# Performance work log

Hardware: AMD Instinct MI355X
Metric: run time of the kernel (lower is better)

The kernel has to match this reference:

```python
import jax, jax.numpy as jnp
import numpy as np

HID = 512; HH = HID // 2; INP = 1; OUT = 1
INH = int(HID * 0.3); EXC = HID - INH            # 153 / 359
N = 3 * HH + 2 * HID + INP                       # 1793 total units
ALM_EXC_START = 3 * HH + HID                      # start of ALM excitatory block
T_CONST = 0.1; SIGMA_REC = 0.01
B, T = 128, 300


def _np_masks():
    rng = np.random.default_rng(0)
    n_zeros = int(np.ceil(0.9 * HH))
    sparse = np.ones((HH, HH), np.float32)
    for c in range(HH):
        sparse[rng.permutation(HH)[:n_zeros], c] = 0.0
    alm2str = np.concatenate([np.ones((HH, EXC), np.float32), np.zeros((HH, INH), np.float32)], 1)
    thal2d1 = np.concatenate([np.ones((HH // 2, HID), np.float32), np.zeros((HH // 2, HID), np.float32)], 0)
    alm2d1 = 1.0 - thal2d1
    iti2d1 = np.concatenate([np.ones((HH // 2, INP), np.float32), np.zeros((HH // 2, INP), np.float32)], 0)
    alm_sign = np.concatenate([np.ones(EXC, np.float32), -np.ones(INH, np.float32)])  # alm2alm_D diagonal
    return sparse, alm2str, thal2d1, alm2d1, iti2d1, alm_sign

_SPARSE, _ALM2STR, _THAL2D1M, _ALM2D1M, _ITI2D1M, _ALMSIGN = [jnp.asarray(a) for a in _np_masks()]


def _clip(w):
    return jnp.clip(w, 1e-10, 1.0)               # F.hardtanh(w, 1e-10, 1)


def _build_W(d12d1_w, d12d2_w, d22d1_w, d22d2_w, d22stn_w, d12thal_w, stn2thal_w,
             thal2alm_w, alm2alm_w, thal2d1_w, thal2d2_w, alm2d1_w, alm2d2_w,
             inp_w_d1, inp_w_d2):
    z_ss = jnp.zeros((HH, HH)); z_sl = jnp.zeros((HH, HID))
    z_ls = jnp.zeros((HID, HH)); z_ll = jnp.zeros((HID, HID))
    z_si = jnp.zeros((HH, INP)); z_li = jnp.zeros((HID, INP))
    # striatal recurrence: sparse_mask * hardtanh(w) @ (-I)
    d12d1 = -(_SPARSE * _clip(d12d1_w)); d12d2 = -(_SPARSE * _clip(d12d2_w))
    d22d1 = -(_SPARSE * _clip(d22d1_w)); d22d2 = -(_SPARSE * _clip(d22d2_w))
    row_d1 = jnp.concatenate([d12d1, d22d1, z_ss, _THAL2D1M * _clip(thal2d1_w),
                              _ALM2D1M * _ALM2STR * _clip(alm2d1_w), _ITI2D1M * _clip(inp_w_d1)], 1)
    row_d2 = jnp.concatenate([d12d2, d22d2, z_ss, _clip(thal2d2_w),
                              _ALM2STR * _clip(alm2d2_w), _clip(inp_w_d2)], 1)
    row_stn = jnp.concatenate([z_ss, _clip(d22stn_w), z_ss, z_sl, z_sl, z_si], 1)
    row_thal = jnp.concatenate([_clip(d12thal_w), z_ls, -_clip(stn2thal_w), z_ll, z_ll, z_li], 1)  # stn2thal @ (-I)
    row_alm = jnp.concatenate([z_ls, z_ls, z_ls, _clip(thal2alm_w),
                               _clip(alm2alm_w) * _ALMSIGN[None, :], z_li], 1)      # alm2alm @ D (Dale)
    row_iti = jnp.zeros((INP, N))
    return jnp.concatenate([row_d1, row_d2, row_stn, row_thal, row_alm, row_iti], 0)


def setup_inputs() -> dict:
    key = jax.random.key(0)
    ks = jax.random.split(key, 24)
    u = lambda k, s: jax.random.uniform(k, s, jnp.float32) * 0.01   # uniform(0, 0.01) init
    return {
        "inp": jax.random.uniform(ks[0], (B, T, INP), jnp.float32),
        "cue_inp": jax.random.uniform(ks[1], (B, T, INP), jnp.float32),
        "inhib_stim": jnp.zeros((B, T, N), jnp.float32),
        "hn": jax.random.uniform(ks[2], (1, B, N), jnp.float32),
        "xn": jax.random.uniform(ks[3], (1, B, N), jnp.float32),
        "noise": jax.random.normal(ks[4], (B, T, N), jnp.float32),
        "d12d1_w": u(ks[5], (HH, HH)), "d12d2_w": u(ks[6], (HH, HH)),
        "d22d1_w": u(ks[7], (HH, HH)), "d22d2_w": u(ks[8], (HH, HH)),
        "d22stn_w": u(ks[9], (HH, HH)), "d12thal_w": u(ks[10], (HID, HH)),
        "stn2thal_w": u(ks[11], (HID, HH)), "thal2alm_w": u(ks[12], (HID, HID)),
        "alm2alm_w": u(ks[13], (HID, HID)), "thal2d1_w": u(ks[14], (HH, HID)),
        "thal2d2_w": u(ks[15], (HH, HID)), "alm2d1_w": u(ks[16], (HH, HID)),
        "alm2d2_w": u(ks[17], (HH, HID)), "inp_w_d1": u(ks[18], (HH, INP)),
        "inp_w_d2": u(ks[19], (HH, INP)), "out_w_alm": u(ks[20], (OUT, EXC)),
    }


def reference(inp, cue_inp, inhib_stim, hn, xn, noise,
              d12d1_w, d12d2_w, d22d1_w, d22d2_w, d22stn_w, d12thal_w, stn2thal_w,
              thal2alm_w, alm2alm_w, thal2d1_w, thal2d2_w, alm2d1_w, alm2d2_w,
              inp_w_d1, inp_w_d2, out_w_alm):
    W = _build_W(d12d1_w, d12d2_w, d22d1_w, d22d2_w, d22stn_w, d12thal_w, stn2thal_w,
                 thal2alm_w, alm2alm_w, thal2d1_w, thal2d2_w, alm2d1_w, alm2d2_w,
                 inp_w_d1, inp_w_d2)
    # tonic current: 0.1 everywhere except ITI units
    tonic = jnp.concatenate([0.1 * jnp.ones(N - INP, jnp.float32), jnp.zeros(INP, jnp.float32)])
    seq = (inhib_stim.swapaxes(0, 1),                 # [T, B, N]
           (inp + cue_inp).swapaxes(0, 1),            # [T, B, INP] -> injected into ITI units
           noise.swapaxes(0, 1))                      # [T, B, N]

    def step(carry, s):
        x, h = carry
        inh_t, iti_t, noise_t = s
        drive = h @ W.T + tonic + inh_t + SIGMA_REC * noise_t
        drive = drive.at[:, N - INP:].add(iti_t)
        x = x + T_CONST * (-x + drive)
        h = jax.nn.relu(x)
        out = h[:, ALM_EXC_START:ALM_EXC_START + EXC] @ out_w_alm.T
        return (x, h), (h, x, out)

    (_, _), (hs, xs, outs) = jax.lax.scan(step, (xn[0], hn[0]), seq)
    return hs.swapaxes(0, 1), xs.swapaxes(0, 1), outs.swapaxes(0, 1)
```

## Files before the change

### kernel.cpp

```cpp
#include <hip/hip_runtime.h>
#include <stdint.h>
#include <string.h>

#define NREAL 1793
#define NPAD  1824
#define NROWP 1808
#define WSTR  1832
#define NBLK  113
#define NGRP  2
#define TSTEPS 300
#define BATCH 128
#define XS_OFF 68851200
#define OUT_OFF 137702400
#define LOFF (16 * WSTR)
#define LOSCALE 4096.0f
#define LOINV  2.44140625e-4f

#define ASLOT(g,i)    (((g) * 128 + (i)) * 32)

typedef _Float16 half_t;
typedef __attribute__((ext_vector_type(8))) _Float16 half8;
typedef __attribute__((ext_vector_type(4))) float f32x4;
typedef __attribute__((ext_vector_type(4))) unsigned int uint4v;

__device__ __forceinline__ float clipw(float w) {
  return fminf(fmaxf(w, 1e-10f), 1.0f);
}

__device__ __forceinline__ void store_u32_llc(unsigned int* p, unsigned int v) {
  asm volatile("global_store_dword %0, %1, off sc0 sc1"
               :: "v"((unsigned long long)(uintptr_t)p), "v"(v)
               : "memory");
}

__device__ __forceinline__ float unpack_h(uint32_t p) {
  unsigned short uh = (unsigned short)(p & 0xffffu);
  unsigned short ul = (unsigned short)(p >> 16);
  half_t hh = *(half_t*)&uh;
  half_t hl = *(half_t*)&ul;
  return (float)hh + LOINV * (float)hl;
}

__device__ __forceinline__ int rid_of(int s) {
  return (s < 8) ? 0 : (s < 16) ? 1 : (s < 32) ? 2 : (s < 48) ? 3
       : (s < 80) ? 4 : (s < 112) ? 5 : 6;
}

__device__ __forceinline__ void poll_wait(unsigned int* cnt, int g, int lane,
                                          bool in0, bool in1, bool cn0, bool cn1,
                                          unsigned tin, unsigned tcn)
{
  const int s0 = lane, s1 = lane + 64;
  for (;;) {
    unsigned a0 = __hip_atomic_load(&cnt[ASLOT(g, s0)], __ATOMIC_RELAXED,
                                    __HIP_MEMORY_SCOPE_AGENT);
    unsigned a1 = 0xFFFFFFFFu;
    if (in1 || cn1)
      a1 = __hip_atomic_load(&cnt[ASLOT(g, s1)], __ATOMIC_RELAXED,
                             __HIP_MEMORY_SCOPE_AGENT);
    unsigned vin = in0 ? a0 : 0xFFFFFFFFu;
    if (in1 && a1 < vin) vin = a1;
    unsigned vcn = cn0 ? a0 : 0xFFFFFFFFu;
    if (cn1 && a1 < vcn) vcn = a1;
    #pragma unroll
    for (int o = 32; o; o >>= 1) {
      unsigned x = __shfl_xor(vin, o); if (x < vin) vin = x;
      unsigned y = __shfl_xor(vcn, o); if (y < vcn) vcn = y;
    }
    if (vin >= tin && vcn >= tcn) break;
    __builtin_amdgcn_s_sleep(1);
  }
}

template<int LO0, int N0, int LO1, int N1, int LO2, int N2>
__device__ __forceinline__ void seg_mfma(const uint32_t* __restrict__ ap,
                                         const half_t* __restrict__ Wl, int wl_b,
                                         f32x4& acc0, f32x4& acc1, f32x4& acc2)
{
  constexpr int NC = N0 + N1 + N2;
  if constexpr (NC == 0) { return; }
  constexpr int BS = 8;
  constexpr int NB = (NC + BS - 1) / BS;
  uint4v qa0[BS], qa1[BS], qb0[BS], qb1[BS];

#define KC_OF(ci) ((ci) < N0 ? (LO0 + (ci)) : (ci) < N0 + N1 ? (LO1 + (ci) - N0) \
                              : (LO2 + (ci) - N0 - N1))

  #pragma unroll
  for (int i = 0; i < BS; ++i) {
    if (i < NC) {
      const int kc = KC_OF(i);
      qa0[i] = *(const uint4v*)(ap + kc * 32);
      qa1[i] = *(const uint4v*)(ap + kc * 32 + 4);
    }
  }
  #pragma unroll
  for (int j = 0; j < NB; ++j) {
    if (j + 1 < NB) {
      #pragma unroll
      for (int i = 0; i < BS; ++i) {
        const int ci = (j + 1) * BS + i;
        if (ci < NC) {
          const int kc = KC_OF(ci);
          if (j % 2 == 0) {
            qb0[i] = *(const uint4v*)(ap + kc * 32);
            qb1[i] = *(const uint4v*)(ap + kc * 32 + 4);
          } else {
            qa0[i] = *(const uint4v*)(ap + kc * 32);
            qa1[i] = *(const uint4v*)(ap + kc * 32 + 4);
          }
        }
      }
    }
    #pragma unroll
    for (int i = 0; i < BS; ++i) {
      const int ci = j * BS + i;
      if (ci < NC) {
        const int kc = KC_OF(ci);
        uint4v v0 = (j % 2 == 0) ? qa0[i] : qb0[i];
        uint4v v1 = (j % 2 == 0) ? qa1[i] : qb1[i];
        uint4v uh, ul;
        uh.x = __builtin_amdgcn_perm(v0.y, v0.x, 0x05040100u);
        uh.y = __builtin_amdgcn_perm(v0.w, v0.z, 0x05040100u);
        uh.z = __builtin_amdgcn_perm(v1.y, v1.x, 0x05040100u);
        uh.w = __builtin_amdgcn_perm(v1.w, v1.z, 0x05040100u);
        ul.x = __builtin_amdgcn_perm(v0.y, v0.x, 0x07060302u);
        ul.y = __builtin_amdgcn_perm(v0.w, v0.z, 0x07060302u);
        ul.z = __builtin_amdgcn_perm(v1.y, v1.x, 0x07060302u);
        ul.w = __builtin_amdgcn_perm(v1.w, v1.z, 0x07060302u);
        union { uint4v u; half8 h; } ch, cl;
        ch.u = uh; cl.u = ul;
        half8 bvh = *(const half8*)&Wl[wl_b + kc * 32];
        half8 bvl = *(const half8*)&Wl[LOFF + wl_b + kc * 32];
        acc0 = __builtin_amdgcn_mfma_f32_16x16x32_f16(ch.h, bvh, acc0, 0, 0, 0);
        acc1 = __builtin_amdgcn_mfma_f32_16x16x32_f16(ch.h, bvl, acc1, 0, 0, 0);
        acc2 = __builtin_amdgcn_mfma_f32_16x16x32_f16(cl.h, bvh, acc2, 0, 0, 0);
      }
    }
  }
#undef KC_OF
}

__global__ __launch_bounds__(256)
void build_w(const float* __restrict__ d12d1, const float* __restrict__ d12d2,
             const float* __restrict__ d22d1, const float* __restrict__ d22d2,
             const float* __restrict__ d22stn, const float* __restrict__ d12thal,
             const float* __restrict__ stn2thal, const float* __restrict__ thal2alm,
             const float* __restrict__ alm2alm, const float* __restrict__ thal2d1,
             const float* __restrict__ thal2d2, const float* __restrict__ alm2d1,
             const float* __restrict__ alm2d2, const float* __restrict__ inpw1,
             const float* __restrict__ inpw2, const unsigned int* __restrict__ mbits,
             half_t* __restrict__ W)
{
  int idx = blockIdx.x * 256 + threadIdx.x;
  if (idx >= NROWP * NPAD) return;
  int i = idx / NPAD, j = idx - (idx / NPAD) * NPAD;
  float v = 0.f;
  if (i < NREAL && j < NREAL) {
    if (i < 256) {
      if (j < 512) {
        int jj = j & 255;
        unsigned bit = (mbits[(i << 3) + (jj >> 5)] >> (jj & 31)) & 1u;
        float wv = (j < 256) ? d12d1[(i << 8) + jj] : d22d1[(i << 8) + jj];
        v = bit ? -clipw(wv) : 0.f;
      } else if (j < 768) {
      } else if (j < 1280) {
        if (i < 128) v = clipw(thal2d1[(i << 9) + (j - 768)]);
      } else if (j < 1792) {
        int jj = j - 1280;
        if (i >= 128 && jj < 359) v = clipw(alm2d1[(i << 9) + jj]);
      } else {
        if (i < 128) v = clipw(inpw1[i]);
      }
    } else if (i < 512) {
      int ii = i - 256;
      if (j < 512) {
        int jj = j & 255;
        unsigned bit = (mbits[(ii << 3) + (jj >> 5)] >> (jj & 31)) & 1u;
        float wv = (j < 256) ? d12d2[(ii << 8) + jj] : d22d2[(ii << 8) + jj];
        v = bit ? -clipw(wv) : 0.f;
      } else if (j < 768) {
      } else if (j < 1280) {
        v = clipw(thal2d2[(ii << 9) + (j - 768)]);
      } else if (j < 1792) {
        int jj = j - 1280;
        if (jj < 359) v = clipw(alm2d2[(ii << 9) + jj]);
      } else {
        v = clipw(inpw2[ii]);
      }
    } else if (i < 768) {
      int ii = i - 512;
      if (j >= 256 && j < 512) v = clipw(d22stn[(ii << 8) + (j - 256)]);
    } else if (i < 1280) {
      int ii = i - 768;
      if (j < 256) v = clipw(d12thal[(ii << 8) + j]);
      else if (j >= 512 && j < 768) v = -clipw(stn2thal[(ii << 8) + (j - 512)]);
    } else if (i < 1792) {
      int ii = i - 1280;
      if (j >= 768 && j < 1280) v = clipw(thal2alm[(ii << 9) + (j - 768)]);
      else if (j >= 1280) {
        int jj = j - 1280;
        v = clipw(alm2alm[(ii << 9) + jj]) * ((jj < 359) ? 1.f : -1.f);
      }
    }
  }
  half_t vh = (half_t)v;
  half_t vl = (half_t)((v - (float)vh) * LOSCALE);
  W[idx] = vh;
  W[(size_t)NROWP * NPAD + idx] = vl;
}

__global__ __launch_bounds__(256)
void init_h(const float* __restrict__ hn, uint32_t* __restrict__ hbuf)
{
  const size_t P4 = (size_t)BATCH * NPAD;
  int idx = blockIdx.x * 256 + threadIdx.x;
  if (idx >= BATCH * NPAD) return;
  int b = idx / NPAD, k = idx - b * NPAD;
  float v = (k < NREAL) ? hn[b * NREAL + k] : 0.f;
  half_t vh = (half_t)v;
  half_t vl = (half_t)((v - (float)vh) * LOSCALE);
  uint32_t hp = (uint32_t)(*(unsigned short*)&vh) |
                ((uint32_t)(*(unsigned short*)&vl) << 16);
  hbuf[idx]      = hp;
  hbuf[P4 + idx] = 0u;
}

__global__ __launch_bounds__(256, 1)
void rnn_step_all(const half_t* __restrict__ Wg, uint32_t* __restrict__ hbuf,
                  unsigned int* __restrict__ cnt,
                  const float* __restrict__ inp, const float* __restrict__ cue,
                  const float* __restrict__ inhib, const float* __restrict__ noise,
                  const float* __restrict__ xn, const float* __restrict__ outw,
                  float* __restrict__ dout)
{
  __shared__ __align__(16) half_t Wl[2 * 16 * WSTR];
  const int tid = threadIdx.x;
  const int bid = blockIdx.x;
  const int g  = bid / NBLK;
  const int nb = bid - g * NBLK;
  const int r0 = nb * 16;
  const int bg = g * 64;
  const size_t P4 = (size_t)BATCH * NPAD;

  const int lane = tid & 63;
  const int w    = tid >> 6;
  const int n_i  = lane & 15;
  const int kq   = lane >> 4;
  const int row  = r0 + n_i;
  const bool valid = row < NREAL;
  const int b0 = bg + 16 * w + kq * 4;
  const int bA = bg + 16 * w + n_i;
  const int wl_b = n_i * WSTR + kq * 8;
  const bool is_outblk = (r0 == 512);
  const bool poll_wave = (tid < 64);

  const int myrid = rid_of(nb);
  const unsigned INB =
      (myrid == 0) ? 87u : (myrid == 1) ? 39u : (myrid == 2) ? 119u :
      (myrid == 3) ? ((nb == 32) ? 36u : 4u) :
      (myrid == 4) ? 11u : (myrid == 5) ? 48u : 0u;
  const unsigned CONSB =
      (myrid <= 1) ? 23u : (myrid == 2) ? 15u : (myrid == 3) ? 16u :
      (myrid == 4) ? 37u : (myrid == 5) ? 46u : 5u;
  const int s1 = lane + 64;
  const int rid0 = rid_of(lane);
  const int rid1 = (s1 < NBLK) ? rid_of(s1) : 6;
  const bool in0 = (lane != nb) && ((INB >> rid0) & 1);
  const bool in1 = (s1 < NBLK) && (s1 != nb) && ((INB >> rid1) & 1);
  const bool cn0 = ((CONSB >> rid0) & 1);
  const bool cn1 = (s1 < NBLK) && ((CONSB >> rid1) & 1);

  float inh[4], noi[4];
  #pragma unroll
  for (int r = 0; r < 4; ++r) {
    inh[r] = 0.f; noi[r] = 0.f;
    if (valid) {
      int ei = ((b0 + r) * TSTEPS) * NREAL + row;
      inh[r] = __builtin_nontemporal_load(&inhib[ei]);
      noi[r] = __builtin_nontemporal_load(&noise[ei]);
    }
  }

  for (int idx = tid; idx < 2 * 16 * (NPAD / 8); idx += 256) {
    int p   = idx / (16 * (NPAD / 8));
    int rem = idx - p * 16 * (NPAD / 8);
    int rr  = rem / (NPAD / 8);
    int cc  = (rem - rr * (NPAD / 8)) * 8;
    *(uint4v*)&Wl[p * LOFF + rr * WSTR + cc] =
        *(const uint4v*)&Wg[(size_t)p * NROWP * NPAD + (size_t)(r0 + rr) * NPAD + cc];
  }
  __syncthreads();

  float xr[4];
  #pragma unroll
  for (int r = 0; r < 4; ++r)
    xr[r] = valid ? xn[(size_t)(b0 + r) * NREAL + row] : 0.f;

  const float tonic = (valid && row < 1792) ? 0.1f : 0.f;
  const bool is_iti = (row == 1792);

  const int ob    = bg + 16 * w + (lane >> 2);
  const int opart = lane & 3;
  const int ou0   = opart * 90;
  const int onu   = (opart == 3) ? 89 : 90;

  #pragma unroll 1
  for (int t = 0; t < TSTEPS; ++t) {
    if (t >= 1) {
      if (poll_wave) {
        poll_wait(cnt, g, lane, in0, in1, cn0, cn1,
                  (unsigned)t, (t >= 2) ? (unsigned)(t - 2) : 0u);
        __builtin_amdgcn_fence(__ATOMIC_ACQUIRE, "agent");
        asm volatile("s_waitcnt vmcnt(0)" ::: "memory");
      }
      __builtin_amdgcn_s_barrier();
      asm volatile("" ::: "memory");
    }

    const uint32_t* hr = hbuf + (size_t)(t & 3) * P4;
    uint32_t*       hw = hbuf + (size_t)((t + 1) & 3) * P4;

    float itv[4];
    #pragma unroll
    for (int r = 0; r < 4; ++r) {
      int bt = (b0 + r) * TSTEPS + t;
      itv[r] = is_iti ? (inp[bt] + cue[bt]) : 0.f;
    }

    const uint32_t* ap = hr + (size_t)bA * NPAD + kq * 8;
    f32x4 acc0 = {0.f, 0.f, 0.f, 0.f};
    f32x4 acc1 = {0.f, 0.f, 0.f, 0.f};
    f32x4 acc2 = {0.f, 0.f, 0.f, 0.f};

    if      (r0 < 128)  seg_mfma<0, 16, 24, 16, 56, 1>(ap, Wl, wl_b, acc0, acc1, acc2);
    else if (r0 < 256)  seg_mfma<0, 16, 40, 12,  0, 0>(ap, Wl, wl_b, acc0, acc1, acc2);
    else if (r0 < 512)  seg_mfma<0, 16, 24, 28, 56, 1>(ap, Wl, wl_b, acc0, acc1, acc2);
    else if (r0 < 768)  seg_mfma<8,  8,  0,  0,  0, 0>(ap, Wl, wl_b, acc0, acc1, acc2);
    else if (r0 < 1280) seg_mfma<0,  8, 16,  8,  0, 0>(ap, Wl, wl_b, acc0, acc1, acc2);
    else if (r0 < 1792) seg_mfma<24, 32, 0,  0,  0, 0>(ap, Wl, wl_b, acc0, acc1, acc2);

    #pragma unroll
    for (int r = 0; r < 4; ++r) {
      float drive = acc0[r] + LOINV * (acc1[r] + acc2[r])
                    + tonic + inh[r] + 0.01f * noi[r] + itv[r];
      float xv = xr[r] + 0.1f * (drive - xr[r]);
      float hv = fmaxf(xv, 0.f);
      xr[r] = xv;
      int bt = (b0 + r) * TSTEPS + t;
      if (valid) {
        int ei = bt * NREAL + row;
        __builtin_nontemporal_store(hv, &dout[ei]);
        __builtin_nontemporal_store(xv, &dout[XS_OFF + ei]);
      }
      half_t hh = (half_t)hv;
      half_t hl = (half_t)((hv - (float)hh) * LOSCALE);
      uint32_t hp = (uint32_t)(*(unsigned short*)&hh) |
                    ((uint32_t)(*(unsigned short*)&hl) << 16);
      store_u32_llc(&hw[(size_t)(b0 + r) * NPAD + row], hp);
    }

    if (is_outblk && t >= 1) {
      const uint32_t* hb = hr + (size_t)ob * NPAD + 1280 + ou0;
      float s = 0.f;
      #pragma unroll 10
      for (int i = 0; i < onu; ++i)
        s += unpack_h(hb[i]) * outw[ou0 + i];
      s += __shfl_xor(s, 1);
      s += __shfl_xor(s, 2);
      if (opart == 0)
        __builtin_nontemporal_store(s, &dout[OUT_OFF + ob * TSTEPS + (t - 1)]);
    }

    if (t + 1 < TSTEPS) {
      #pragma unroll
      for (int r = 0; r < 4; ++r) {
        if (valid) {
          int ei = ((b0 + r) * TSTEPS + (t + 1)) * NREAL + row;
          inh[r] = __builtin_nontemporal_load(&inhib[ei]);
          noi[r] = __builtin_nontemporal_load(&noise[ei]);
        }
      }
      asm volatile("s_waitcnt vmcnt(8)" ::: "memory");
    } else {
      asm volatile("s_waitcnt vmcnt(0)" ::: "memory");
    }
    __builtin_amdgcn_s_barrier();
    if (tid == 0)
      store_u32_llc(&cnt[ASLOT(g, nb)], (unsigned)(t + 1));
  }

  if (is_outblk) {
    if (poll_wave) {
      poll_wait(cnt, g, lane, in0, in1, false, false, (unsigned)TSTEPS, 0u);
      __builtin_amdgcn_fence(__ATOMIC_ACQUIRE, "agent");
      asm volatile("s_waitcnt vmcnt(0)" ::: "memory");
    }
    __builtin_amdgcn_s_barrier();
    asm volatile("" ::: "memory");
    const uint32_t* hr = hbuf + (size_t)(TSTEPS & 3) * P4;
    const uint32_t* hb = hr + (size_t)ob * NPAD + 1280 + ou0;
    float s = 0.f;
    #pragma unroll 10
    for (int i = 0; i < onu; ++i)
      s += unpack_h(hb[i]) * outw[ou0 + i];
    s += __shfl_xor(s, 1);
    s += __shfl_xor(s, 2);
    if (opart == 0)
      __builtin_nontemporal_store(s, &dout[OUT_OFF + ob * TSTEPS + (TSTEPS - 1)]);
  }
}

static void compute_sparse_mask(uint32_t* mb) {
  uint32_t pool[4];
  uint32_t hc = 0x43b0d7e5u;
  auto hashmix = [&hc](uint32_t value) -> uint32_t {
    value ^= hc; hc *= 0x931e8875u; value *= hc; value ^= value >> 16; return value;
  };
  auto mixf = [](uint32_t x, uint32_t y) -> uint32_t {
    uint32_t r = x * 0xca01f9ddu;
    r -= y * 0x4973f715u;
    r ^= r >> 16;
    return r;
  };
  for (int i = 0; i < 4; ++i) pool[i] = hashmix(0u);
  for (int s = 0; s < 4; ++s)
    for (int d = 0; d < 4; ++d)
      if (s != d) pool[d] = mixf(pool[d], hashmix(pool[s]));
  uint32_t st[8];
  uint32_t hb = 0x8b51f9ddu;
  for (int i = 0; i < 8; ++i) {
    uint32_t dv = pool[i & 3];
    dv ^= hb; hb *= 0x58f38dedu; dv *= hb; dv ^= dv >> 16;
    st[i] = dv;
  }
  uint64_t v64[4];
  for (int i = 0; i < 4; ++i) v64[i] = (uint64_t)st[2 * i] | ((uint64_t)st[2 * i + 1] << 32);
  typedef unsigned __int128 u128;
  const u128 MULT = ((u128)0x2360ed051fc65da4ULL << 64) | 0x4385df649fccf645ULL;
  u128 initstate = ((u128)v64[0] << 64) | v64[1];
  u128 initseq   = ((u128)v64[2] << 64) | v64[3];
  u128 state = 0, inc = (initseq << 1) | 1;
  state = state * MULT + inc;
  state += initstate;
  state = state * MULT + inc;
  bool has32 = false; uint32_t cached = 0;
  auto next64 = [&]() -> uint64_t {
    state = state * MULT + inc;
    uint64_t hi = (uint64_t)(state >> 64), lo = (uint64_t)state;
    unsigned rot = (unsigned)(state >> 122);
    uint64_t x = hi ^ lo;
    return (x >> rot) | (x << ((64 - rot) & 63));
  };
  auto next32 = [&]() -> uint32_t {
    if (has32) { has32 = false; return cached; }
    uint64_t v = next64();
    has32 = true; cached = (uint32_t)(v >> 32);
    return (uint32_t)v;
  };
  auto rinterval = [&](uint32_t mx) -> uint32_t {
    if (mx == 0) return 0;
    uint32_t mask = mx;
    mask |= mask >> 1; mask |= mask >> 2; mask |= mask >> 4;
    mask |= mask >> 8; mask |= mask >> 16;
    uint32_t value;
    do { value = next32() & mask; } while (value > mx);
    return value;
  };
  for (int i = 0; i < 256 * 8; ++i) mb[i] = 0xFFFFFFFFu;
  int perm[256];
  for (int c = 0; c < 256; ++c) {
    for (int i = 0; i < 256; ++i) perm[i] = i;
    for (int i = 255; i >= 1; --i) {
      uint32_t j = rinterval((uint32_t)i);
      int tmp = perm[i]; perm[i] = perm[j]; perm[j] = tmp;
    }
    for (int z = 0; z < 231; ++z)
      mb[perm[z] * 8 + (c >> 5)] &= ~(1u << (c & 31));
  }
}

extern "C" void kernel_launch(void* const* d_in, const int* in_sizes, int n_in,
                              void* d_out, int out_size, void* d_ws, size_t ws_size,
                              hipStream_t stream)
{
  (void)in_sizes; (void)n_in; (void)out_size; (void)ws_size;
  const float* inp   = (const float*)d_in[0];
  const float* cue   = (const float*)d_in[1];
  const float* inhib = (const float*)d_in[2];
  const float* hn    = (const float*)d_in[3];
  const float* xn    = (const float*)d_in[4];
  const float* noise = (const float*)d_in[5];
  const float* outw  = (const float*)d_in[21];
  float* dout = (float*)d_out;

  char* ws = (char*)d_ws;
  const size_t W_BYTES = (size_t)2 * NROWP * NPAD * sizeof(half_t);
  const size_t H_BYTES = (size_t)4 * BATCH * NPAD * 4;
  half_t*   W    = (half_t*)ws;
  uint32_t* hbuf = (uint32_t*)(ws + W_BYTES);
  unsigned int* mbits = (unsigned int*)(ws + W_BYTES + H_BYTES);
  unsigned int* cnt   = (unsigned int*)(ws + W_BYTES + H_BYTES + 32768);

  static uint32_t hmask[256 * 8];
  compute_sparse_mask(hmask);
  (void)hipMemcpyAsync(mbits, hmask, sizeof(hmask), hipMemcpyHostToDevice, stream);
  (void)hipMemsetAsync(cnt, 0, 32768, stream);

  build_w<<<(NROWP * NPAD + 255) / 256, 256, 0, stream>>>(
      (const float*)d_in[6],  (const float*)d_in[7],  (const float*)d_in[8],
      (const float*)d_in[9],  (const float*)d_in[10], (const float*)d_in[11],
      (const float*)d_in[12], (const float*)d_in[13], (const float*)d_in[14],
      (const float*)d_in[15], (const float*)d_in[16], (const float*)d_in[17],
      (const float*)d_in[18], (const float*)d_in[19], (const float*)d_in[20],
      mbits, W);
  init_h<<<(BATCH * NPAD + 255) / 256, 256, 0, stream>>>(hn, hbuf);

  void* args[] = {(void*)&W, (void*)&hbuf, (void*)&cnt, (void*)&inp, (void*)&cue,
                  (void*)&inhib, (void*)&noise, (void*)&xn, (void*)&outw, (void*)&dout};
  hipError_t err = hipLaunchCooperativeKernel(reinterpret_cast<void*>(rnn_step_all),
                                              dim3(NGRP * NBLK), dim3(256), args, 0, stream);
  if (err != hipSuccess) {
    rnn_step_all<<<dim3(NGRP * NBLK), dim3(256), 0, stream>>>(
        W, hbuf, cnt, inp, cue, inhib, noise, xn, outw, dout);
  }
}
```

Baseline: 3.902 ms.

## Replace persistent cooperative kernel with one launch per timestep

Drops the persistent cooperative kernel, whose blocks synchronised through per-block counters and dependency-aware polling. Each of the 300 timesteps is now its own kernel launch, with the x state kept in a global buffer and h ping-ponged between two buffers. This removes the polling and spin-wait logic. In exchange, every step pays a kernel launch, reloads the weight tile into shared memory, and loses the overlap between steps.

```diff
diff --git a/kernel.cpp b/kernel.cpp
--- a/kernel.cpp
+++ b/kernel.cpp
@@ -16,8 +16,6 @@
 #define LOSCALE 4096.0f
 #define LOINV  2.44140625e-4f
 
-#define ASLOT(g,i)    (((g) * 128 + (i)) * 32)
-
 typedef _Float16 half_t;
 typedef __attribute__((ext_vector_type(8))) _Float16 half8;
 typedef __attribute__((ext_vector_type(4))) float f32x4;
@@ -25,12 +23,6 @@
 
 __device__ __forceinline__ float clipw(float w) {
   return fminf(fmaxf(w, 1e-10f), 1.0f);
-}
-
-__device__ __forceinline__ void store_u32_llc(unsigned int* p, unsigned int v) {
-  asm volatile("global_store_dword %0, %1, off sc0 sc1"
-               :: "v"((unsigned long long)(uintptr_t)p), "v"(v)
-               : "memory");
 }
 
 __device__ __forceinline__ float unpack_h(uint32_t p) {
@@ -41,37 +33,6 @@
   return (float)hh + LOINV * (float)hl;
 }
 
-__device__ __forceinline__ int rid_of(int s) {
-  return (s < 8) ? 0 : (s < 16) ? 1 : (s < 32) ? 2 : (s < 48) ? 3
-       : (s < 80) ? 4 : (s < 112) ? 5 : 6;
-}
-
-__device__ __forceinline__ void poll_wait(unsigned int* cnt, int g, int lane,
-                                          bool in0, bool in1, bool cn0, bool cn1,
-                                          unsigned tin, unsigned tcn)
-{
-  const int s0 = lane, s1 = lane + 64;
-  for (;;) {
-    unsigned a0 = __hip_atomic_load(&cnt[ASLOT(g, s0)], __ATOMIC_RELAXED,
-                                    __HIP_MEMORY_SCOPE_AGENT);
-    unsigned a1 = 0xFFFFFFFFu;
-    if (in1 || cn1)
-      a1 = __hip_atomic_load(&cnt[ASLOT(g, s1)], __ATOMIC_RELAXED,
-                             __HIP_MEMORY_SCOPE_AGENT);
-    unsigned vin = in0 ? a0 : 0xFFFFFFFFu;
-    if (in1 && a1 < vin) vin = a1;
-    unsigned vcn = cn0 ? a0 : 0xFFFFFFFFu;
-    if (cn1 && a1 < vcn) vcn = a1;
-    #pragma unroll
-    for (int o = 32; o; o >>= 1) {
-      unsigned x = __shfl_xor(vin, o); if (x < vin) vin = x;
-      unsigned y = __shfl_xor(vcn, o); if (y < vcn) vcn = y;
-    }
-    if (vin >= tin && vcn >= tcn) break;
-    __builtin_amdgcn_s_sleep(1);
-  }
-}
-
 template<int LO0, int N0, int LO1, int N1, int LO2, int N2>
 __device__ __forceinline__ void seg_mfma(const uint32_t* __restrict__ ap,
                                          const half_t* __restrict__ Wl, int wl_b,
@@ -85,7 +46,6 @@
 
 #define KC_OF(ci) ((ci) < N0 ? (LO0 + (ci)) : (ci) < N0 + N1 ? (LO1 + (ci) - N0) \
                               : (LO2 + (ci) - N0 - N1))
-
   #pragma unroll
   for (int i = 0; i < BS; ++i) {
     if (i < NC) {
@@ -211,28 +171,30 @@
 }
 
 __global__ __launch_bounds__(256)
-void init_h(const float* __restrict__ hn, uint32_t* __restrict__ hbuf)
+void init_hx(const float* __restrict__ hn, const float* __restrict__ xn,
+             uint32_t* __restrict__ hbuf, float* __restrict__ xbuf)
 {
   const size_t P4 = (size_t)BATCH * NPAD;
   int idx = blockIdx.x * 256 + threadIdx.x;
   if (idx >= BATCH * NPAD) return;
   int b = idx / NPAD, k = idx - b * NPAD;
-  float v = (k < NREAL) ? hn[b * NREAL + k] : 0.f;
-  half_t vh = (half_t)v;
-  half_t vl = (half_t)((v - (float)vh) * LOSCALE);
+  float hv = (k < NREAL) ? hn[b * NREAL + k] : 0.f;
+  float xv = (k < NREAL) ? xn[b * NREAL + k] : 0.f;
+  half_t vh = (half_t)hv;
+  half_t vl = (half_t)((hv - (float)vh) * LOSCALE);
   uint32_t hp = (uint32_t)(*(unsigned short*)&vh) |
                 ((uint32_t)(*(unsigned short*)&vl) << 16);
   hbuf[idx]      = hp;
   hbuf[P4 + idx] = 0u;
+  xbuf[idx]      = xv;
 }
 
 __global__ __launch_bounds__(256, 1)
-void rnn_step_all(const half_t* __restrict__ Wg, uint32_t* __restrict__ hbuf,
-                  unsigned int* __restrict__ cnt,
-                  const float* __restrict__ inp, const float* __restrict__ cue,
-                  const float* __restrict__ inhib, const float* __restrict__ noise,
-                  const float* __restrict__ xn, const float* __restrict__ outw,
-                  float* __restrict__ dout)
+void rnn_step(const half_t* __restrict__ Wg, uint32_t* __restrict__ hbuf,
+              float* __restrict__ xbuf,
+              const float* __restrict__ inp, const float* __restrict__ cue,
+              const float* __restrict__ inhib, const float* __restrict__ noise,
+              const float* __restrict__ outw, float* __restrict__ dout, int t)
 {
   __shared__ __align__(16) half_t Wl[2 * 16 * WSTR];
   const int tid = threadIdx.x;
@@ -253,33 +215,20 @@
   const int bA = bg + 16 * w + n_i;
   const int wl_b = n_i * WSTR + kq * 8;
   const bool is_outblk = (r0 == 512);
-  const bool poll_wave = (tid < 64);
-
-  const int myrid = rid_of(nb);
-  const unsigned INB =
-      (myrid == 0) ? 87u : (myrid == 1) ? 39u : (myrid == 2) ? 119u :
-      (myrid == 3) ? ((nb == 32) ? 36u : 4u) :
-      (myrid == 4) ? 11u : (myrid == 5) ? 48u : 0u;
-  const unsigned CONSB =
-      (myrid <= 1) ? 23u : (myrid == 2) ? 15u : (myrid == 3) ? 16u :
-      (myrid == 4) ? 37u : (myrid == 5) ? 46u : 5u;
-  const int s1 = lane + 64;
-  const int rid0 = rid_of(lane);
-  const int rid1 = (s1 < NBLK) ? rid_of(s1) : 6;
-  const bool in0 = (lane != nb) && ((INB >> rid0) & 1);
-  const bool in1 = (s1 < NBLK) && (s1 != nb) && ((INB >> rid1) & 1);
-  const bool cn0 = ((CONSB >> rid0) & 1);
-  const bool cn1 = (s1 < NBLK) && ((CONSB >> rid1) & 1);
-
-  float inh[4], noi[4];
+  const bool is_iti = (row == 1792);
+
+  float inh[4], noi[4], itv[4], xr[4];
   #pragma unroll
   for (int r = 0; r < 4; ++r) {
     inh[r] = 0.f; noi[r] = 0.f;
+    int bt = (b0 + r) * TSTEPS + t;
     if (valid) {
-      int ei = ((b0 + r) * TSTEPS) * NREAL + row;
+      int ei = bt * NREAL + row;
       inh[r] = __builtin_nontemporal_load(&inhib[ei]);
       noi[r] = __builtin_nontemporal_load(&noise[ei]);
     }
+    itv[r] = is_iti ? (inp[bt] + cue[bt]) : 0.f;
+    xr[r] = xbuf[(size_t)(b0 + r) * NPAD + row];
   }
 
   for (int idx = tid; idx < 2 * 16 * (NPAD / 8); idx += 256) {
@@ -292,113 +241,47 @@
   }
   __syncthreads();
 
-  float xr[4];
+  const uint32_t* hr = hbuf + (size_t)(t & 1) * P4;
+  uint32_t*       hw = hbuf + (size_t)((t + 1) & 1) * P4;
+
+  const uint32_t* ap = hr + (size_t)bA * NPAD + kq * 8;
+  f32x4 acc0 = {0.f, 0.f, 0.f, 0.f};
+  f32x4 acc1 = {0.f, 0.f, 0.f, 0.f};
+  f32x4 acc2 = {0.f, 0.f, 0.f, 0.f};
+
+  if      (r0 < 128)  seg_mfma<0, 16, 24, 16, 56, 1>(ap, Wl, wl_b, acc0, acc1, acc2);
+  else if (r0 < 256)  seg_mfma<0, 16, 40, 12,  0, 0>(ap, Wl, wl_b, acc0, acc1, acc2);
+  else if (r0 < 512)  seg_mfma<0, 16, 24, 28, 56, 1>(ap, Wl, wl_b, acc0, acc1, acc2);
+  else if (r0 < 768)  seg_mfma<8,  8,  0,  0,  0, 0>(ap, Wl, wl_b, acc0, acc1, acc2);
+  else if (r0 < 1280) seg_mfma<0,  8, 16,  8,  0, 0>(ap, Wl, wl_b, acc0, acc1, acc2);
+  else if (r0 < 1792) seg_mfma<24, 32, 0,  0,  0, 0>(ap, Wl, wl_b, acc0, acc1, acc2);
+
+  const float tonic = (valid && row < 1792) ? 0.1f : 0.f;
   #pragma unroll
-  for (int r = 0; r < 4; ++r)
-    xr[r] = valid ? xn[(size_t)(b0 + r) * NREAL + row] : 0.f;
-
-  const float tonic = (valid && row < 1792) ? 0.1f : 0.f;
-  const bool is_iti = (row == 1792);
-
-  const int ob    = bg + 16 * w + (lane >> 2);
-  const int opart = lane & 3;
-  const int ou0   = opart * 90;
-  const int onu   = (opart == 3) ? 89 : 90;
-
-  #pragma unroll 1
-  for (int t = 0; t < TSTEPS; ++t) {
-    if (t >= 1) {
-      if (poll_wave) {
-        poll_wait(cnt, g, lane, in0, in1, cn0, cn1,
-                  (unsigned)t, (t >= 2) ? (unsigned)(t - 2) : 0u);
-        __builtin_amdgcn_fence(__ATOMIC_ACQUIRE, "agent");
-        asm volatile("s_waitcnt vmcnt(0)" ::: "memory");
-      }
-      __builtin_amdgcn_s_barrier();
-      asm volatile("" ::: "memory");
-    }
-
-    const uint32_t* hr = hbuf + (size_t)(t & 3) * P4;
-    uint32_t*       hw = hbuf + (size_t)((t + 1) & 3) * P4;
-
-    float itv[4];
-    #pragma unroll
-    for (int r = 0; r < 4; ++r) {
-      int bt = (b0 + r) * TSTEPS + t;
-      itv[r] = is_iti ? (inp[bt] + cue[bt]) : 0.f;
-    }
-
-    const uint32_t* ap = hr + (size_t)bA * NPAD + kq * 8;
-    f32x4 acc0 = {0.f, 0.f, 0.f, 0.f};
-    f32x4 acc1 = {0.f, 0.f, 0.f, 0.f};
-    f32x4 acc2 = {0.f, 0.f, 0.f, 0.f};
-
-    if      (r0 < 128)  seg_mfma<0, 16, 24, 16, 56, 1>(ap, Wl, wl_b, acc0, acc1, acc2);
-    else if (r0 < 256)  seg_mfma<0, 16, 40, 12,  0, 0>(ap, Wl, wl_b, acc0, acc1, acc2);
-    else if (r0 < 512)  seg_mfma<0, 16, 24, 28, 56, 1>(ap, Wl, wl_b, acc0, acc1, acc2);
-    else if (r0 < 768)  seg_mfma<8,  8,  0,  0,  0, 0>(ap, Wl, wl_b, acc0, acc1, acc2);
-    else if (r0 < 1280) seg_mfma<0,  8, 16,  8,  0, 0>(ap, Wl, wl_b, acc0, acc1, acc2);
-    else if (r0 < 1792) seg_mfma<24, 32, 0,  0,  0, 0>(ap, Wl, wl_b, acc0, acc1, acc2);
-
-    #pragma unroll
-    for (int r = 0; r < 4; ++r) {
-      float drive = acc0[r] + LOINV * (acc1[r] + acc2[r])
-                    + tonic + inh[r] + 0.01f * noi[r] + itv[r];
-      float xv = xr[r] + 0.1f * (drive - xr[r]);
-      float hv = fmaxf(xv, 0.f);
-      xr[r] = xv;
-      int bt = (b0 + r) * TSTEPS + t;
-      if (valid) {
-        int ei = bt * NREAL + row;
-        __builtin_nontemporal_store(hv, &dout[ei]);
-        __builtin_nontemporal_store(xv, &dout[XS_OFF + ei]);
-      }
-      half_t hh = (half_t)hv;
-      half_t hl = (half_t)((hv - (float)hh) * LOSCALE);
-      uint32_t hp = (uint32_t)(*(unsigned short*)&hh) |
-                    ((uint32_t)(*(unsigned short*)&hl) << 16);
-      store_u32_llc(&hw[(size_t)(b0 + r) * NPAD + row], hp);
-    }
-
-    if (is_outblk && t >= 1) {
-      const uint32_t* hb = hr + (size_t)ob * NPAD + 1280 + ou0;
-      float s = 0.f;
-      #pragma unroll 10
-      for (int i = 0; i < onu; ++i)
-        s += unpack_h(hb[i]) * outw[ou0 + i];
-      s += __shfl_xor(s, 1);
-      s += __shfl_xor(s, 2);
-      if (opart == 0)
-        __builtin_nontemporal_store(s, &dout[OUT_OFF + ob * TSTEPS + (t - 1)]);
-    }
-
-    if (t + 1 < TSTEPS) {
-      #pragma unroll
-      for (int r = 0; r < 4; ++r) {
-        if (valid) {
-          int ei = ((b0 + r) * TSTEPS + (t + 1)) * NREAL + row;
-          inh[r] = __builtin_nontemporal_load(&inhib[ei]);
-          noi[r] = __builtin_nontemporal_load(&noise[ei]);
-        }
-      }
-      asm volatile("s_waitcnt vmcnt(8)" ::: "memory");
-    } else {
-      asm volatile("s_waitcnt vmcnt(0)" ::: "memory");
-    }
-    __builtin_amdgcn_s_barrier();
-    if (tid == 0)
-      store_u32_llc(&cnt[ASLOT(g, nb)], (unsigned)(t + 1));
-  }
-
-  if (is_outblk) {
-    if (poll_wave) {
-      poll_wait(cnt, g, lane, in0, in1, false, false, (unsigned)TSTEPS, 0u);
-      __builtin_amdgcn_fence(__ATOMIC_ACQUIRE, "agent");
-      asm volatile("s_waitcnt vmcnt(0)" ::: "memory");
-    }
-    __builtin_amdgcn_s_barrier();
-    asm volatile("" ::: "memory");
-    const uint32_t* hr = hbuf + (size_t)(TSTEPS & 3) * P4;
+  for (int r = 0; r < 4; ++r) {
+    float drive = acc0[r] + LOINV * (acc1[r] + acc2[r])
+                  + tonic + inh[r] + 0.01f * noi[r] + itv[r];
+    float xv = xr[r] + 0.1f * (drive - xr[r]);
+    float hv = fmaxf(xv, 0.f);
+    int bt = (b0 + r) * TSTEPS + t;
+    if (valid) {
+      int ei = bt * NREAL + row;
+      __builtin_nontemporal_store(hv, &dout[ei]);
+      __builtin_nontemporal_store(xv, &dout[XS_OFF + ei]);
+    }
+    half_t hh = (half_t)hv;
+    half_t hl = (half_t)((hv - (float)hh) * LOSCALE);
+    uint32_t hp = (uint32_t)(*(unsigned short*)&hh) |
+                  ((uint32_t)(*(unsigned short*)&hl) << 16);
+    hw[(size_t)(b0 + r) * NPAD + row] = hp;
+    xbuf[(size_t)(b0 + r) * NPAD + row] = xv;
+  }
+
+  if (is_outblk && t >= 1) {
+    const int ob    = bg + 16 * w + (lane >> 2);
+    const int opart = lane & 3;
+    const int ou0   = opart * 90;
+    const int onu   = (opart == 3) ? 89 : 90;
     const uint32_t* hb = hr + (size_t)ob * NPAD + 1280 + ou0;
     float s = 0.f;
     #pragma unroll 10
@@ -407,8 +290,32 @@
     s += __shfl_xor(s, 1);
     s += __shfl_xor(s, 2);
     if (opart == 0)
-      __builtin_nontemporal_store(s, &dout[OUT_OFF + ob * TSTEPS + (TSTEPS - 1)]);
-  }
+      __builtin_nontemporal_store(s, &dout[OUT_OFF + ob * TSTEPS + (t - 1)]);
+  }
+}
+
+__global__ __launch_bounds__(256)
+void out_final(const uint32_t* __restrict__ hbuf, const float* __restrict__ outw,
+               float* __restrict__ dout)
+{
+  const int g = blockIdx.x;
+  const int tid = threadIdx.x;
+  const int lane = tid & 63;
+  const int w = tid >> 6;
+  const int ob    = g * 64 + 16 * w + (lane >> 2);
+  const int opart = lane & 3;
+  const int ou0   = opart * 90;
+  const int onu   = (opart == 3) ? 89 : 90;
+  const uint32_t* hr = hbuf + (size_t)(TSTEPS & 1) * BATCH * NPAD;
+  const uint32_t* hb = hr + (size_t)ob * NPAD + 1280 + ou0;
+  float s = 0.f;
+  #pragma unroll 10
+  for (int i = 0; i < onu; ++i)
+    s += unpack_h(hb[i]) * outw[ou0 + i];
+  s += __shfl_xor(s, 1);
+  s += __shfl_xor(s, 2);
+  if (opart == 0)
+    dout[OUT_OFF + ob * TSTEPS + (TSTEPS - 1)] = s;
 }
 
 static void compute_sparse_mask(uint32_t* mb) {
@@ -496,16 +403,16 @@
 
   char* ws = (char*)d_ws;
   const size_t W_BYTES = (size_t)2 * NROWP * NPAD * sizeof(half_t);
-  const size_t H_BYTES = (size_t)4 * BATCH * NPAD * 4;
+  const size_t H_BYTES = (size_t)2 * BATCH * NPAD * 4;
+  const size_t X_BYTES = (size_t)BATCH * NPAD * 4;
   half_t*   W    = (half_t*)ws;
   uint32_t* hbuf = (uint32_t*)(ws + W_BYTES);
-  unsigned int* mbits = (unsigned int*)(ws + W_BYTES + H_BYTES);
-  unsigned int* cnt   = (unsigned int*)(ws + W_BYTES + H_BYTES + 32768);
+  float*    xbuf = (float*)(ws + W_BYTES + H_BYTES);
+  unsigned int* mbits = (unsigned int*)(ws + W_BYTES + H_BYTES + X_BYTES);
 
   static uint32_t hmask[256 * 8];
   compute_sparse_mask(hmask);
   (void)hipMemcpyAsync(mbits, hmask, sizeof(hmask), hipMemcpyHostToDevice, stream);
-  (void)hipMemsetAsync(cnt, 0, 32768, stream);
 
   build_w<<<(NROWP * NPAD + 255) / 256, 256, 0, stream>>>(
       (const float*)d_in[6],  (const float*)d_in[7],  (const float*)d_in[8],
@@ -514,14 +421,11 @@
       (const float*)d_in[15], (const float*)d_in[16], (const float*)d_in[17],
       (const float*)d_in[18], (const float*)d_in[19], (const float*)d_in[20],
       mbits, W);
-  init_h<<<(BATCH * NPAD + 255) / 256, 256, 0, stream>>>(hn, hbuf);
-
-  void* args[] = {(void*)&W, (void*)&hbuf, (void*)&cnt, (void*)&inp, (void*)&cue,
-                  (void*)&inhib, (void*)&noise, (void*)&xn, (void*)&outw, (void*)&dout};
-  hipError_t err = hipLaunchCooperativeKernel(reinterpret_cast<void*>(rnn_step_all),
-                                              dim3(NGRP * NBLK), dim3(256), args, 0, stream);
-  if (err != hipSuccess) {
-    rnn_step_all<<<dim3(NGRP * NBLK), dim3(256), 0, stream>>>(
-        W, hbuf, cnt, inp, cue, inhib, noise, xn, outw, dout);
-  }
-}
+  init_hx<<<(BATCH * NPAD + 255) / 256, 256, 0, stream>>>(hn, xn, hbuf, xbuf);
+
+  for (int t = 0; t < TSTEPS; ++t) {
+    rnn_step<<<dim3(NGRP * NBLK), dim3(256), 0, stream>>>(
+        W, hbuf, xbuf, inp, cue, inhib, noise, outw, dout, t);
+  }
+  out_final<<<dim3(2), dim3(256), 0, stream>>>(hbuf, outw, dout);
+}
```

Measured after the change: 7.127 ms. +82.6%, slower.
